# Kernel tuning notes

Hardware: AMD Instinct MI355X
Metric: run time of the kernel (lower is better)

## Reference

```python
import jax, jax.numpy as jnp
import numpy as np

EPS = 1e-12  # matches torch F.normalize eps


def _l2n(x, axis):
    return x / jnp.maximum(jnp.linalg.norm(x, axis=axis, keepdims=True), EPS)


def setup_inputs() -> dict:
    key = jax.random.key(0)
    k1, k2, k3 = jax.random.split(key, 3)
    x = jax.random.normal(k1, (4, 128, 30, 40), dtype=jnp.float32)
    conv_w = jax.random.normal(k2, (64, 128), dtype=jnp.float32) * 0.02  # 1x1 conv, no bias (vladv2=False)
    centroids = jax.random.uniform(k3, (64, 128), dtype=jnp.float32)
    return {"x": x, "conv_w": conv_w, "centroids": centroids}


def reference(x, conv_w, centroids):
    N, C, H, W = x.shape
    K = centroids.shape[0]
    ps, stride = 4, 1  # patch_sizes='4', strides='1'

    # descriptor-wise L2 normalization of input
    x = _l2n(x, 1)

    # 1x1 conv + softmax over clusters -> soft assignment [N,K,H,W]
    soft_assign = jax.nn.softmax(jnp.einsum('kc,nchw->nkhw', conv_w, x), axis=1)

    # weighted residuals [N,K,C,H,W] (vectorized form of the per-cluster loop)
    res = (x[:, None] - centroids[None, :, :, None, None]) * soft_assign[:, :, None]

    # global VLAD: sum over spatial, intra-norm, flatten, L2-norm
    vlad_global = res.sum(axis=(-1, -2))            # [N,K,C]
    vlad_global = _l2n(vlad_global, 2).reshape(N, K * C)
    vlad_global = _l2n(vlad_global, 1)

    # integral image over spatial dims with zero pad on top/left
    r = res.reshape(N, K * C, H, W)
    integ = jnp.cumsum(jnp.cumsum(r, axis=-1), axis=-2)
    integ = jnp.pad(integ, ((0, 0), (0, 0), (1, 0), (1, 0)))  # [N,KC,H+1,W+1]

    # dilated 2x2 box-filter conv == 4-corner integral-image lookup
    TL = integ[:, :, :H + 1 - ps:stride, :W + 1 - ps:stride]
    TR = integ[:, :, :H + 1 - ps:stride, ps::stride]
    BL = integ[:, :, ps::stride, :W + 1 - ps:stride]
    BR = integ[:, :, ps::stride, ps::stride]
    vl = (TL - TR - BL + BR) / (ps * ps)            # [N,KC,Hp,Wp]
    Hp, Wp = vl.shape[-2], vl.shape[-1]

    # local VLAD: intra-norm over descriptor dim, then global L2 per patch
    vl = vl.reshape(N, K, C, Hp * Wp)
    vl = _l2n(vl, 2).reshape(N, K * C, Hp * Wp)
    vlad_local = _l2n(vl, 1)

    return vlad_global, vlad_local
```

## Files before the change

kernel.cpp:

```cpp
#include <hip/hip_runtime.h>
#include <math.h>

#define EPSV 1e-12f

namespace {
constexpr int N_  = 4;
constexpr int C_  = 128;
constexpr int H_  = 30;
constexpr int W_  = 40;
constexpr int K_  = 64;
constexpr int HW_ = H_ * W_;
constexpr int HP_ = 27;
constexpr int WP_ = 37;
constexpr int P_  = HP_ * WP_;
constexpr int PS_ = 1000;
constexpr int KC_ = K_ * C_;
constexpr int CP_ = C_ * P_;
constexpr int CS_ = HP_ * W_;
constexpr int SL_ = CS_ / 4;
constexpr int CVP_ = 132;
}

static __device__ __forceinline__ float4 ld4(const float* p) {
    return *reinterpret_cast<const float4*>(p);
}
static __device__ __forceinline__ float dot4(float4 a, float4 b) {
    return a.x * b.x + a.y * b.y + a.z * b.z + a.w * b.w;
}
static __device__ __forceinline__ float4 f4add(float4 a, float4 b) {
    return make_float4(a.x + b.x, a.y + b.y, a.z + b.z, a.w + b.w);
}

__global__ __launch_bounds__(256) void k1_norm_softmax(
    const float* __restrict__ x, const float* __restrict__ conv_w,
    float* __restrict__ xnT, float* __restrict__ xnP, float* __restrict__ sa)
{
    __shared__ float xrow[C_ * W_];
    __shared__ float conv_s[K_ * CVP_];
    __shared__ float xrowT[W_ * CVP_];
    __shared__ float invn[W_];
    __shared__ float s_s[K_ * W_];

    const int b = blockIdx.x;
    const int n = b / H_, h = b - n * H_;
    const int t = threadIdx.x;

    for (int i = t; i < C_ * W_; i += 256) {
        const int c = i / W_, w = i - c * W_;
        xrow[i] = x[(size_t)(n * C_ + c) * HW_ + h * W_ + w];
    }
    for (int i = t; i < K_ * C_; i += 256) {
        const int k = i >> 7, c = i & 127;
        conv_s[k * CVP_ + c] = conv_w[i];
    }
    __syncthreads();

    if (t < W_) {
        float s = 0.f;
        for (int c = 0; c < C_; ++c) { const float v = xrow[c * W_ + t]; s += v * v; }
        invn[t] = 1.f / fmaxf(sqrtf(s), EPSV);
    }
    __syncthreads();

    for (int i = t; i < C_ * W_; i += 256) {
        const int c = i / W_, w = i - c * W_;
        const float v = xrow[i] * invn[w];
        xrow[i] = v;
        xnT[(size_t)(n * C_ + c) * HW_ + h * W_ + w] = v;
    }
    __syncthreads();

    for (int i = t; i < W_ * C_; i += 256) {
        const int w = i / C_, c = i - w * C_;
        const float v = xrow[c * W_ + w];
        xnP[((size_t)n * HW_ + h * W_ + w) * C_ + c] = v;
        xrowT[w * CVP_ + c] = v;
    }
    __syncthreads();

    {
        const int k = t >> 2, q = t & 3;
        float acc0 = 0.f, acc1 = 0.f, acc2 = 0.f, acc3 = 0.f, acc4 = 0.f;
        float acc5 = 0.f, acc6 = 0.f, acc7 = 0.f, acc8 = 0.f, acc9 = 0.f;
        const float* convk = &conv_s[k * CVP_];
        for (int ch = 0; ch < 4; ++ch) {
            float4 cv0 = ld4(convk + ch * 32 + 0),  cv1 = ld4(convk + ch * 32 + 4);
            float4 cv2 = ld4(convk + ch * 32 + 8),  cv3 = ld4(convk + ch * 32 + 12);
            float4 cv4 = ld4(convk + ch * 32 + 16), cv5 = ld4(convk + ch * 32 + 20);
            float4 cv6 = ld4(convk + ch * 32 + 24), cv7 = ld4(convk + ch * 32 + 28);
#pragma unroll
            for (int wi = 0; wi < 10; ++wi) {
                const float* xw = &xrowT[(q * 10 + wi) * CVP_ + ch * 32];
                float s = dot4(cv0, ld4(xw)) + dot4(cv1, ld4(xw + 4))
                        + dot4(cv2, ld4(xw + 8)) + dot4(cv3, ld4(xw + 12))
                        + dot4(cv4, ld4(xw + 16)) + dot4(cv5, ld4(xw + 20))
                        + dot4(cv6, ld4(xw + 24)) + dot4(cv7, ld4(xw + 28));
                if      (wi == 0) acc0 += s; else if (wi == 1) acc1 += s;
                else if (wi == 2) acc2 += s; else if (wi == 3) acc3 += s;
                else if (wi == 4) acc4 += s; else if (wi == 5) acc5 += s;
                else if (wi == 6) acc6 += s; else if (wi == 7) acc7 += s;
                else if (wi == 8) acc8 += s; else              acc9 += s;
            }
        }
        float* sd = &s_s[k * W_ + q * 10];
        sd[0] = acc0; sd[1] = acc1; sd[2] = acc2; sd[3] = acc3; sd[4] = acc4;
        sd[5] = acc5; sd[6] = acc6; sd[7] = acc7; sd[8] = acc8; sd[9] = acc9;
    }
    __syncthreads();

    if (t < W_) {
        const int w = t;
        float m = -1e30f;
        for (int k = 0; k < K_; ++k) m = fmaxf(m, s_s[k * W_ + w]);
        float sum = 0.f;
        for (int k = 0; k < K_; ++k) sum += expf(s_s[k * W_ + w] - m);
        const float inv = 1.f / sum;
        for (int k = 0; k < K_; ++k)
            sa[(size_t)(n * K_ + k) * HW_ + h * W_ + w] = expf(s_s[k * W_ + w] - m) * inv;
    }
}

#define COLSUM_VEC_T(cs_q, sa_s, x0, x1, x2, x3)                                \
    for (int s = t; s < SL_; s += 256) {                                        \
        const int i = s * 4;                                                    \
        const float4 sa0 = ld4(&sa_s[i]);                                       \
        const float4 sa1 = ld4(&sa_s[i + W_]);                                  \
        const float4 sa2 = ld4(&sa_s[i + 2 * W_]);                              \
        const float4 sa3 = ld4(&sa_s[i + 3 * W_]);                              \
        float acc[4][4];                                                        \
        const float* xc[4] = {x0, x1, x2, x3};                                  \
        _Pragma("unroll")                                                       \
        for (int ch = 0; ch < 4; ++ch) {                                        \
            const float4 a0 = ld4(xc[ch] + i);                                  \
            const float4 a1 = ld4(xc[ch] + i + W_);                             \
            const float4 a2 = ld4(xc[ch] + i + 2 * W_);                         \
            const float4 a3 = ld4(xc[ch] + i + 3 * W_);                         \
            acc[0][ch] = sa0.x * a0.x + sa1.x * a1.x + sa2.x * a2.x + sa3.x * a3.x; \
            acc[1][ch] = sa0.y * a0.y + sa1.y * a1.y + sa2.y * a2.y + sa3.y * a3.y; \
            acc[2][ch] = sa0.z * a0.z + sa1.z * a1.z + sa2.z * a2.z + sa3.z * a3.z; \
            acc[3][ch] = sa0.w * a0.w + sa1.w * a1.w + sa2.w * a2.w + sa3.w * a3.w; \
        }                                                                       \
        _Pragma("unroll")                                                       \
        for (int q = 0; q < 4; ++q)                                             \
            cs_q[q][s] = make_float4(acc[q][0], acc[q][1], acc[q][2], acc[q][3]); \
    }

#define WINDOW10(cs_q, b0, d, A0, A1, A2, A3)                                   \
    {                                                                           \
        float4 v0 = cs_q[(b0 + 0) & 3][(b0 + 0) >> 2];                          \
        float4 v1 = cs_q[(b0 + 1) & 3][(b0 + 1) >> 2];                          \
        float4 v2 = cs_q[(b0 + 2) & 3][(b0 + 2) >> 2];                          \
        float4 v3 = cs_q[(b0 + 3) & 3][(b0 + 3) >> 2];                          \
        float4 v4 = cs_q[(b0 + 4) & 3][(b0 + 4) >> 2];                          \
        float4 v5 = cs_q[(b0 + 5) & 3][(b0 + 5) >> 2];                          \
        float4 v6 = cs_q[(b0 + 6) & 3][(b0 + 6) >> 2];                          \
        float4 v7 = cs_q[(b0 + 7) & 3][(b0 + 7) >> 2];                          \
        float4 v8 = cs_q[(b0 + 8) & 3][(b0 + 8) >> 2];                          \
        float4 v9 = cs_q[(b0 + 9) & 3][(b0 + 9) >> 2];                          \
        const float4 t0 = f4add(v0, v1), t1 = f4add(v1, v2), t2 = f4add(v2, v3);\
        const float4 t3 = f4add(v3, v4), t4 = f4add(v4, v5), t5 = f4add(v5, v6);\
        const float4 t6 = f4add(v6, v7), t7 = f4add(v7, v8), t8 = f4add(v8, v9);\
        const float4 w0 = f4add(t0, t2), w1 = f4add(t1, t3), w2 = f4add(t2, t4);\
        const float4 w3 = f4add(t3, t5), w4 = f4add(t4, t6), w5 = f4add(t5, t7);\
        const float4 w6 = f4add(t6, t8);                                        \
        A0 = (0 < d) ? w0 : w3;                                                 \
        A1 = (1 < d) ? w1 : w4;                                                 \
        A2 = (2 < d) ? w2 : w5;                                                 \
        A3 = (3 < d) ? w3 : w6;                                                 \
    }

__global__ __launch_bounds__(256) void k4_merged(
    const float* __restrict__ sa, const float* __restrict__ xnT,
    const float* __restrict__ xnP, const float* __restrict__ cent,
    float* __restrict__ nsqp, float* __restrict__ vg_u,
    float* __restrict__ vg_r)
{
    __shared__ float  sa_s[HW_ + 8];
    __shared__ float4 cs_q[4][SL_ + 1];
    __shared__ float  gs[256], bss[256];
    __shared__ float  red[2];

    const int t = threadIdx.x;

    if (blockIdx.x < 256) {
        const int b = blockIdx.x;
        const int n = b >> 6, k = b & 63;
        const int c = t & 127, half = t >> 7;
        constexpr int HHW = HW_ / 2;

        const float* sarow = &sa[(size_t)b * HW_ + half * HHW];
        const float* xp = &xnP[((size_t)n * HW_ + half * HHW) * C_ + c];
        float g0 = 0.f, g1 = 0.f, g2 = 0.f, g3 = 0.f;
        float b0 = 0.f, b1 = 0.f, b2 = 0.f, b3 = 0.f;
        for (int pix = 0; pix < HHW; pix += 4) {
            const float s0 = sarow[pix + 0], s1 = sarow[pix + 1];
            const float s2 = sarow[pix + 2], s3 = sarow[pix + 3];
            g0 += s0 * xp[(size_t)(pix + 0) * C_];
            g1 += s1 * xp[(size_t)(pix + 1) * C_];
            g2 += s2 * xp[(size_t)(pix + 2) * C_];
            g3 += s3 * xp[(size_t)(pix + 3) * C_];
            b0 += s0; b1 += s1; b2 += s2; b3 += s3;
        }
        gs[t]  = (g0 + g1) + (g2 + g3);
        bss[t] = (b0 + b1) + (b2 + b3);
        __syncthreads();

        float vg = 0.f;
        if (t < 128) {
            vg = (gs[t] + gs[t + 128]) - cent[k * C_ + c] * (bss[t] + bss[t + 128]);
            float nsq = vg * vg;
            for (int off = 32; off >= 1; off >>= 1) nsq += __shfl_down(nsq, off);
            if ((t & 63) == 0) red[t >> 6] = nsq;
        }
        __syncthreads();
        const float tot  = red[0] + red[1];
        const float norm = sqrtf(tot);
        const float iv   = 1.f / fmaxf(norm, EPSV);
        if (t < 128) vg_u[(size_t)b * C_ + t] = vg * iv;
        if (t == 0) { const float rr = norm * iv; vg_r[b] = rr * rr; }
        return;
    }

    const int b  = blockIdx.x - 256;
    const int cq = b & 3;
    const int nk = b >> 2;
    const int n  = nk >> 6, k = nk & 63;

    for (int i = t; i < HW_; i += 256) sa_s[i] = sa[(size_t)nk * HW_ + i];
    __syncthreads();

    int hp0 = 0, b0 = 0, d = 4;
    float B0 = 0.f, B1 = 0.f, B2 = 0.f, B3 = 0.f;
    if (t < 250) {
        const int p0 = 4 * t;
        hp0 = p0 / WP_;
        const int wp0 = p0 - hp0 * WP_;
        b0 = p0 + 3 * hp0;
        d  = WP_ - wp0;
        const float* r0 = &sa_s[hp0 * W_ + wp0];
        float sc[10];
#pragma unroll
        for (int j = 0; j < 10; ++j)
            sc[j] = r0[j] + r0[j + W_] + r0[j + 2 * W_] + r0[j + 3 * W_];
        const float u0 = sc[0] + sc[1], u1 = sc[1] + sc[2], u2 = sc[2] + sc[3];
        const float u3 = sc[3] + sc[4], u4 = sc[4] + sc[5], u5 = sc[5] + sc[6];
        const float u6 = sc[6] + sc[7], u7 = sc[7] + sc[8], u8 = sc[8] + sc[9];
        const float wB0 = u0 + u2, wB1 = u1 + u3, wB2 = u2 + u4;
        const float wB3 = u3 + u5, wB4 = u4 + u6, wB5 = u5 + u7, wB6 = u6 + u8;
        B0 = (0 < d) ? wB0 : wB3;
        B1 = (1 < d) ? wB1 : wB4;
        B2 = (2 < d) ? wB2 : wB5;
        B3 = (3 < d) ? wB3 : wB6;
    }

    float4 nv0 = make_float4(0, 0, 0, 0), nv1 = nv0, nv2 = nv0, nv3 = nv0;
    const float* xb = xnT + (size_t)n * C_ * HW_;

    for (int g = 0; g < 8; ++g) {
        const int c0 = cq * 32 + g * 4;
        const float* x0 = xb + (size_t)(c0 + 0) * HW_;
        const float* x1 = xb + (size_t)(c0 + 1) * HW_;
        const float* x2 = xb + (size_t)(c0 + 2) * HW_;
        const float* x3 = xb + (size_t)(c0 + 3) * HW_;
        __syncthreads();
        COLSUM_VEC_T(cs_q, sa_s, x0, x1, x2, x3)
        __syncthreads();
        if (t < 250) {
            const float4 ce = ld4(&cent[k * C_ + c0]);
            float4 A0, A1, A2, A3;
            WINDOW10(cs_q, b0, d, A0, A1, A2, A3)
            const float4 e0 = make_float4(A0.x - ce.x * B0, A0.y - ce.y * B0,
                                          A0.z - ce.z * B0, A0.w - ce.w * B0);
            const float4 e1 = make_float4(A1.x - ce.x * B1, A1.y - ce.y * B1,
                                          A1.z - ce.z * B1, A1.w - ce.w * B1);
            const float4 e2 = make_float4(A2.x - ce.x * B2, A2.y - ce.y * B2,
                                          A2.z - ce.z * B2, A2.w - ce.w * B2);
            const float4 e3 = make_float4(A3.x - ce.x * B3, A3.y - ce.y * B3,
                                          A3.z - ce.z * B3, A3.w - ce.w * B3);
            nv0 = make_float4(nv0.x + e0.x * e0.x, nv0.y + e0.y * e0.y,
                              nv0.z + e0.z * e0.z, nv0.w + e0.w * e0.w);
            nv1 = make_float4(nv1.x + e1.x * e1.x, nv1.y + e1.y * e1.y,
                              nv1.z + e1.z * e1.z, nv1.w + e1.w * e1.w);
            nv2 = make_float4(nv2.x + e2.x * e2.x, nv2.y + e2.y * e2.y,
                              nv2.z + e2.z * e2.z, nv2.w + e2.w * e2.w);
            nv3 = make_float4(nv3.x + e3.x * e3.x, nv3.y + e3.y * e3.y,
                              nv3.z + e3.z * e3.z, nv3.w + e3.w * e3.w);
        }
    }
    if (t < 250) {
        const float s0 = (nv0.x + nv0.y) + (nv0.z + nv0.w);
        const float s1 = (nv1.x + nv1.y) + (nv1.z + nv1.w);
        const float s2 = (nv2.x + nv2.y) + (nv2.z + nv2.w);
        const float s3 = (nv3.x + nv3.y) + (nv3.z + nv3.w);
        *reinterpret_cast<float4*>(&nsqp[(size_t)b * PS_ + 4 * t]) =
            make_float4(s0 * 0.00390625f, s1 * 0.00390625f,
                        s2 * 0.00390625f, s3 * 0.00390625f);
    }
}

__global__ __launch_bounds__(256) void k5_merged(
    const float* __restrict__ nsqp, float* __restrict__ inv1,
    float* __restrict__ rloc, const float* __restrict__ vg_u,
    const float* __restrict__ vg_r, float* __restrict__ out)
{
    const int t = threadIdx.x;
    if (blockIdx.x >= 256) {
        const int n = blockIdx.x - 256;
        __shared__ float inv2s;
        if (t == 0) {
            float s = 0.f;
            for (int k = 0; k < K_; ++k) s += vg_r[n * K_ + k];
            inv2s = 1.f / fmaxf(sqrtf(s), EPSV);
        }
        __syncthreads();
        const float inv2 = inv2s;
        for (int i = t; i < KC_; i += 256)
            out[(size_t)n * KC_ + i] = vg_u[(size_t)n * KC_ + i] * inv2;
        return;
    }
    const int nk = blockIdx.x;
    if (t < 250) {
        const int p0 = 4 * t;
        const float4 a = ld4(&nsqp[(size_t)(nk * 4 + 0) * PS_ + p0]);
        const float4 b = ld4(&nsqp[(size_t)(nk * 4 + 1) * PS_ + p0]);
        const float4 c = ld4(&nsqp[(size_t)(nk * 4 + 2) * PS_ + p0]);
        const float4 e = ld4(&nsqp[(size_t)(nk * 4 + 3) * PS_ + p0]);
        float4 iv, rr;
#pragma unroll
        for (int j = 0; j < 4; ++j) {
            const float s = reinterpret_cast<const float*>(&a)[j]
                          + reinterpret_cast<const float*>(&b)[j]
                          + reinterpret_cast<const float*>(&c)[j]
                          + reinterpret_cast<const float*>(&e)[j];
            const float norm = sqrtf(s);
            const float v = 1.f / fmaxf(norm, EPSV);
            reinterpret_cast<float*>(&iv)[j] = v * 0.0625f;
            const float r = norm * v;
            reinterpret_cast<float*>(&rr)[j] = r * r;
        }
        *reinterpret_cast<float4*>(&inv1[(size_t)nk * PS_ + p0]) = iv;
        *reinterpret_cast<float4*>(&rloc[(size_t)nk * PS_ + p0]) = rr;
    }
}

__global__ __launch_bounds__(256) void k6_inv2(
    const float* __restrict__ rloc, float* __restrict__ inv2)
{
    const int n = blockIdx.x;
    const int t = threadIdx.x;
    if (t < 250) {
        const int p0 = 4 * t;
        float4 s = make_float4(0, 0, 0, 0);
        for (int k = 0; k < K_; ++k) {
            const float4 r = ld4(&rloc[(size_t)(n * K_ + k) * PS_ + p0]);
            s = f4add(s, r);
        }
        float4 o;
        o.x = 1.f / fmaxf(sqrtf(s.x), EPSV);
        o.y = 1.f / fmaxf(sqrtf(s.y), EPSV);
        o.z = 1.f / fmaxf(sqrtf(s.z), EPSV);
        o.w = 1.f / fmaxf(sqrtf(s.w), EPSV);
        *reinterpret_cast<float4*>(&inv2[n * PS_ + p0]) = o;
    }
}

__global__ __launch_bounds__(256) void k7_write(
    const float* __restrict__ sa, const float* __restrict__ xnT,
    const float* __restrict__ cent, const float* __restrict__ inv1,
    const float* __restrict__ inv2, float* __restrict__ outl)
{
    __shared__ float  sa_s[HW_ + 8];
    __shared__ float  scl_s[P_];
    __shared__ float  t2_s[P_];
    __shared__ float4 cs_q[4][SL_ + 1];

    const int b  = blockIdx.x;
    const int cq = b & 3;
    const int nk = b >> 2;
    const int n  = nk >> 6, k = nk & 63;
    const int t  = threadIdx.x;

    for (int i = t; i < HW_; i += 256) sa_s[i] = sa[(size_t)nk * HW_ + i];
    __syncthreads();
    for (int p = t; p < P_; p += 256) {
        const int hp = p / WP_, wp = p - hp * WP_;
        float bs = 0.f;
#pragma unroll
        for (int dh = 0; dh < 4; ++dh) {
            const float* r = &sa_s[(hp + dh) * W_ + wp];
            bs += r[0] + r[1] + r[2] + r[3];
        }
        const float sc = inv1[(size_t)nk * PS_ + p] * inv2[n * PS_ + p];
        scl_s[p] = sc;
        t2_s[p]  = bs * sc;
    }

    const float* xb = xnT + (size_t)n * C_ * HW_;
    float* ob = outl + (size_t)nk * CP_;

    for (int g = 0; g < 8; ++g) {
        const int m = g & 3, h8 = g >> 2;
        const int c0 = cq * 32 + h8 * 16 + m;
        const float* x0 = xb + (size_t)(c0 + 0) * HW_;
        const float* x1 = xb + (size_t)(c0 + 4) * HW_;
        const float* x2 = xb + (size_t)(c0 + 8) * HW_;
        const float* x3 = xb + (size_t)(c0 + 12) * HW_;
        __syncthreads();
        COLSUM_VEC_T(cs_q, sa_s, x0, x1, x2, x3)
        __syncthreads();
        const float ce0 = cent[k * C_ + c0];
        const float ce1 = cent[k * C_ + c0 + 4];
        const float ce2 = cent[k * C_ + c0 + 8];
        const float ce3 = cent[k * C_ + c0 + 12];
        float* ob0 = ob + (size_t)(c0 + 0) * P_;
        float* ob1 = ob + (size_t)(c0 + 4) * P_;
        float* ob2 = ob + (size_t)(c0 + 8) * P_;
        float* ob3 = ob + (size_t)(c0 + 12) * P_;

        if (t < 249) {
            const int p0 = m + 4 * t;
            const int hp0 = p0 / WP_;
            const int wp0 = p0 - hp0 * WP_;
            const int b0 = p0 + 3 * hp0;
            const int d  = WP_ - wp0;
            const float sc0 = scl_s[p0 + 0], sc1 = scl_s[p0 + 1];
            const float sc2 = scl_s[p0 + 2], sc3 = scl_s[p0 + 3];
            const float tt0 = t2_s[p0 + 0], tt1 = t2_s[p0 + 1];
            const float tt2 = t2_s[p0 + 2], tt3 = t2_s[p0 + 3];
            float4 A0, A1, A2, A3;
            WINDOW10(cs_q, b0, d, A0, A1, A2, A3)
            const float4 s0v = make_float4(A0.x * sc0 - ce0 * tt0, A1.x * sc1 - ce0 * tt1,
                                           A2.x * sc2 - ce0 * tt2, A3.x * sc3 - ce0 * tt3);
            const float4 s1v = make_float4(A0.y * sc0 - ce1 * tt0, A1.y * sc1 - ce1 * tt1,
                                           A2.y * sc2 - ce1 * tt2, A3.y * sc3 - ce1 * tt3);
            const float4 s2v = make_float4(A0.z * sc0 - ce2 * tt0, A1.z * sc1 - ce2 * tt1,
                                           A2.z * sc2 - ce2 * tt2, A3.z * sc3 - ce2 * tt3);
            const float4 s3v = make_float4(A0.w * sc0 - ce3 * tt0, A1.w * sc1 - ce3 * tt1,
                                           A2.w * sc2 - ce3 * tt2, A3.w * sc3 - ce3 * tt3);
            *reinterpret_cast<float4*>(ob0 + p0) = s0v;
            *reinterpret_cast<float4*>(ob1 + p0) = s1v;
            *reinterpret_cast<float4*>(ob2 + p0) = s2v;
            *reinterpret_cast<float4*>(ob3 + p0) = s3v;
        } else if (t < 252) {
            const int u = t - 249;
            const int p = (u < m) ? u : 996 + u;
            const int hp = p / WP_, wp = p - hp * WP_;
            const int base = hp * W_ + wp;
            const float4 s0 = cs_q[(base + 0) & 3][(base + 0) >> 2];
            const float4 s1 = cs_q[(base + 1) & 3][(base + 1) >> 2];
            const float4 s2 = cs_q[(base + 2) & 3][(base + 2) >> 2];
            const float4 s3 = cs_q[(base + 3) & 3][(base + 3) >> 2];
            const float sc = scl_s[p], tt = t2_s[p];
            ob0[p] = (s0.x + s1.x + s2.x + s3.x) * sc - ce0 * tt;
            ob1[p] = (s0.y + s1.y + s2.y + s3.y) * sc - ce1 * tt;
            ob2[p] = (s0.z + s1.z + s2.z + s3.z) * sc - ce2 * tt;
            ob3[p] = (s0.w + s1.w + s2.w + s3.w) * sc - ce3 * tt;
        }
    }
}

extern "C" void kernel_launch(void* const* d_in, const int* in_sizes, int n_in,
                              void* d_out, int out_size, void* d_ws, size_t ws_size,
                              hipStream_t stream)
{
    const float* x      = (const float*)d_in[0];
    const float* conv_w = (const float*)d_in[1];
    const float* cent   = (const float*)d_in[2];
    float* out = (float*)d_out;
    float* ws  = (float*)d_ws;

    float* xnT  = ws;
    float* xnP  = ws + 614400;
    float* sa   = ws + 1228800;
    float* vg_u = ws + 1536000;
    float* vg_r = ws + 1568768;
    float* nsqp = ws + 1569024;
    float* inv1 = ws + 2593024;
    float* rloc = ws + 2849024;
    float* inv2 = ws + 3105024;

    float* outl = out + (size_t)N_ * KC_;

    k1_norm_softmax<<<N_ * H_, 256, 0, stream>>>(x, conv_w, xnT, xnP, sa);
    k4_merged<<<256 + N_ * K_ * 4, 256, 0, stream>>>(sa, xnT, xnP, cent,
                                                     nsqp, vg_u, vg_r);
    k5_merged<<<256 + N_, 256, 0, stream>>>(nsqp, inv1, rloc, vg_u, vg_r, out);
    k6_inv2<<<N_, 256, 0, stream>>>(rloc, inv2);
    k7_write<<<N_ * K_ * 4, 256, 0, stream>>>(sa, xnT, cent, inv1, inv2, outl);
}
```

Before: 120.2 us.

## Replace shared-memory colsum/window passes with per-thread register 2x4 patch tiles

The k4 and k7 box-filter kernels no longer stage soft-assignments and column sums in shared memory with block barriers. Each thread now owns a 2-row by 4-column group of output patches and reads a 5x8 window of sa and xnT straight from global memory into registers, computing the 4x4 box sums locally for each channel in its slice. This removes every __syncthreads and the shared-memory staging, and spreads the work over a flat grid of threads. The cost is redundant overlapping global loads (each input element is read by several threads), possibly uncoalesced unaligned stores, and more register use per thread.

```diff
diff --git a/kernel.cpp b/kernel.cpp
--- a/kernel.cpp
+++ b/kernel.cpp
@@ -16,19 +16,31 @@
 constexpr int PS_ = 1000;
 constexpr int KC_ = K_ * C_;
 constexpr int CP_ = C_ * P_;
-constexpr int CS_ = HP_ * W_;
-constexpr int SL_ = CS_ / 4;
 constexpr int CVP_ = 132;
-}
+constexpr int SLOT_ = 140;
+constexpr int K4S_BLK = 560;
+constexpr int K7_BLK  = 1120;
+}
+
+typedef float4 f4u __attribute__((aligned(4)));
 
 static __device__ __forceinline__ float4 ld4(const float* p) {
     return *reinterpret_cast<const float4*>(p);
 }
+static __device__ __forceinline__ float4 ld4u(const float* p) {
+    return *reinterpret_cast<const f4u*>(p);
+}
+static __device__ __forceinline__ void st4u(float* p, float4 v) {
+    *reinterpret_cast<f4u*>(p) = v;
+}
 static __device__ __forceinline__ float dot4(float4 a, float4 b) {
     return a.x * b.x + a.y * b.y + a.z * b.z + a.w * b.w;
 }
 static __device__ __forceinline__ float4 f4add(float4 a, float4 b) {
     return make_float4(a.x + b.x, a.y + b.y, a.z + b.z, a.w + b.w);
+}
+static __device__ __forceinline__ float4 f4mul(float4 a, float4 b) {
+    return make_float4(a.x * b.x, a.y * b.y, a.z * b.z, a.w * b.w);
 }
 
 __global__ __launch_bounds__(256) void k1_norm_softmax(
@@ -80,8 +92,7 @@
 
     {
         const int k = t >> 2, q = t & 3;
-        float acc0 = 0.f, acc1 = 0.f, acc2 = 0.f, acc3 = 0.f, acc4 = 0.f;
-        float acc5 = 0.f, acc6 = 0.f, acc7 = 0.f, acc8 = 0.f, acc9 = 0.f;
+        float acc[10] = {};
         const float* convk = &conv_s[k * CVP_];
         for (int ch = 0; ch < 4; ++ch) {
             float4 cv0 = ld4(convk + ch * 32 + 0),  cv1 = ld4(convk + ch * 32 + 4);
@@ -91,20 +102,15 @@
 #pragma unroll
             for (int wi = 0; wi < 10; ++wi) {
                 const float* xw = &xrowT[(q * 10 + wi) * CVP_ + ch * 32];
-                float s = dot4(cv0, ld4(xw)) + dot4(cv1, ld4(xw + 4))
-                        + dot4(cv2, ld4(xw + 8)) + dot4(cv3, ld4(xw + 12))
-                        + dot4(cv4, ld4(xw + 16)) + dot4(cv5, ld4(xw + 20))
-                        + dot4(cv6, ld4(xw + 24)) + dot4(cv7, ld4(xw + 28));
-                if      (wi == 0) acc0 += s; else if (wi == 1) acc1 += s;
-                else if (wi == 2) acc2 += s; else if (wi == 3) acc3 += s;
-                else if (wi == 4) acc4 += s; else if (wi == 5) acc5 += s;
-                else if (wi == 6) acc6 += s; else if (wi == 7) acc7 += s;
-                else if (wi == 8) acc8 += s; else              acc9 += s;
+                acc[wi] += dot4(cv0, ld4(xw)) + dot4(cv1, ld4(xw + 4))
+                         + dot4(cv2, ld4(xw + 8)) + dot4(cv3, ld4(xw + 12))
+                         + dot4(cv4, ld4(xw + 16)) + dot4(cv5, ld4(xw + 20))
+                         + dot4(cv6, ld4(xw + 24)) + dot4(cv7, ld4(xw + 28));
             }
         }
         float* sd = &s_s[k * W_ + q * 10];
-        sd[0] = acc0; sd[1] = acc1; sd[2] = acc2; sd[3] = acc3; sd[4] = acc4;
-        sd[5] = acc5; sd[6] = acc6; sd[7] = acc7; sd[8] = acc8; sd[9] = acc9;
+#pragma unroll
+        for (int wi = 0; wi < 10; ++wi) sd[wi] = acc[wi];
     }
     __syncthreads();
 
@@ -120,70 +126,23 @@
     }
 }
 
-#define COLSUM_VEC_T(cs_q, sa_s, x0, x1, x2, x3)                                \
-    for (int s = t; s < SL_; s += 256) {                                        \
-        const int i = s * 4;                                                    \
-        const float4 sa0 = ld4(&sa_s[i]);                                       \
-        const float4 sa1 = ld4(&sa_s[i + W_]);                                  \
-        const float4 sa2 = ld4(&sa_s[i + 2 * W_]);                              \
-        const float4 sa3 = ld4(&sa_s[i + 3 * W_]);                              \
-        float acc[4][4];                                                        \
-        const float* xc[4] = {x0, x1, x2, x3};                                  \
-        _Pragma("unroll")                                                       \
-        for (int ch = 0; ch < 4; ++ch) {                                        \
-            const float4 a0 = ld4(xc[ch] + i);                                  \
-            const float4 a1 = ld4(xc[ch] + i + W_);                             \
-            const float4 a2 = ld4(xc[ch] + i + 2 * W_);                         \
-            const float4 a3 = ld4(xc[ch] + i + 3 * W_);                         \
-            acc[0][ch] = sa0.x * a0.x + sa1.x * a1.x + sa2.x * a2.x + sa3.x * a3.x; \
-            acc[1][ch] = sa0.y * a0.y + sa1.y * a1.y + sa2.y * a2.y + sa3.y * a3.y; \
-            acc[2][ch] = sa0.z * a0.z + sa1.z * a1.z + sa2.z * a2.z + sa3.z * a3.z; \
-            acc[3][ch] = sa0.w * a0.w + sa1.w * a1.w + sa2.w * a2.w + sa3.w * a3.w; \
-        }                                                                       \
-        _Pragma("unroll")                                                       \
-        for (int q = 0; q < 4; ++q)                                             \
-            cs_q[q][s] = make_float4(acc[q][0], acc[q][1], acc[q][2], acc[q][3]); \
-    }
-
-#define WINDOW10(cs_q, b0, d, A0, A1, A2, A3)                                   \
-    {                                                                           \
-        float4 v0 = cs_q[(b0 + 0) & 3][(b0 + 0) >> 2];                          \
-        float4 v1 = cs_q[(b0 + 1) & 3][(b0 + 1) >> 2];                          \
-        float4 v2 = cs_q[(b0 + 2) & 3][(b0 + 2) >> 2];                          \
-        float4 v3 = cs_q[(b0 + 3) & 3][(b0 + 3) >> 2];                          \
-        float4 v4 = cs_q[(b0 + 4) & 3][(b0 + 4) >> 2];                          \
-        float4 v5 = cs_q[(b0 + 5) & 3][(b0 + 5) >> 2];                          \
-        float4 v6 = cs_q[(b0 + 6) & 3][(b0 + 6) >> 2];                          \
-        float4 v7 = cs_q[(b0 + 7) & 3][(b0 + 7) >> 2];                          \
-        float4 v8 = cs_q[(b0 + 8) & 3][(b0 + 8) >> 2];                          \
-        float4 v9 = cs_q[(b0 + 9) & 3][(b0 + 9) >> 2];                          \
-        const float4 t0 = f4add(v0, v1), t1 = f4add(v1, v2), t2 = f4add(v2, v3);\
-        const float4 t3 = f4add(v3, v4), t4 = f4add(v4, v5), t5 = f4add(v5, v6);\
-        const float4 t6 = f4add(v6, v7), t7 = f4add(v7, v8), t8 = f4add(v8, v9);\
-        const float4 w0 = f4add(t0, t2), w1 = f4add(t1, t3), w2 = f4add(t2, t4);\
-        const float4 w3 = f4add(t3, t5), w4 = f4add(t4, t6), w5 = f4add(t5, t7);\
-        const float4 w6 = f4add(t6, t8);                                        \
-        A0 = (0 < d) ? w0 : w3;                                                 \
-        A1 = (1 < d) ? w1 : w4;                                                 \
-        A2 = (2 < d) ? w2 : w5;                                                 \
-        A3 = (3 < d) ? w3 : w6;                                                 \
-    }
-
-__global__ __launch_bounds__(256) void k4_merged(
+static __device__ __forceinline__ float4 win4(float4 a, float4 b) {
+    const float t0 = a.x + a.y, t1 = a.y + a.z, t2 = a.z + a.w;
+    const float t3 = a.w + b.x, t4 = b.x + b.y, t5 = b.y + b.z;
+    return make_float4(t0 + t2, t1 + t3, t2 + t4, t3 + t5);
+}
+
+__global__ __launch_bounds__(256) void k4_flat(
     const float* __restrict__ sa, const float* __restrict__ xnT,
     const float* __restrict__ xnP, const float* __restrict__ cent,
     float* __restrict__ nsqp, float* __restrict__ vg_u,
     float* __restrict__ vg_r)
 {
-    __shared__ float  sa_s[HW_ + 8];
-    __shared__ float4 cs_q[4][SL_ + 1];
-    __shared__ float  gs[256], bss[256];
-    __shared__ float  red[2];
-
+    __shared__ float gs[256], bss[256], red[2];
     const int t = threadIdx.x;
 
-    if (blockIdx.x < 256) {
-        const int b = blockIdx.x;
+    if (blockIdx.x >= K4S_BLK) {
+        const int b = blockIdx.x - K4S_BLK;
         const int n = b >> 6, k = b & 63;
         const int c = t & 127, half = t >> 7;
         constexpr int HHW = HW_ / 2;
@@ -221,80 +180,74 @@
         return;
     }
 
-    const int b  = blockIdx.x - 256;
-    const int cq = b & 3;
-    const int nk = b >> 2;
-    const int n  = nk >> 6, k = nk & 63;
-
-    for (int i = t; i < HW_; i += 256) sa_s[i] = sa[(size_t)nk * HW_ + i];
-    __syncthreads();
-
-    int hp0 = 0, b0 = 0, d = 4;
-    float B0 = 0.f, B1 = 0.f, B2 = 0.f, B3 = 0.f;
-    if (t < 250) {
-        const int p0 = 4 * t;
-        hp0 = p0 / WP_;
-        const int wp0 = p0 - hp0 * WP_;
-        b0 = p0 + 3 * hp0;
-        d  = WP_ - wp0;
-        const float* r0 = &sa_s[hp0 * W_ + wp0];
-        float sc[10];
-#pragma unroll
-        for (int j = 0; j < 10; ++j)
-            sc[j] = r0[j] + r0[j + W_] + r0[j + 2 * W_] + r0[j + 3 * W_];
-        const float u0 = sc[0] + sc[1], u1 = sc[1] + sc[2], u2 = sc[2] + sc[3];
-        const float u3 = sc[3] + sc[4], u4 = sc[4] + sc[5], u5 = sc[5] + sc[6];
-        const float u6 = sc[6] + sc[7], u7 = sc[7] + sc[8], u8 = sc[8] + sc[9];
-        const float wB0 = u0 + u2, wB1 = u1 + u3, wB2 = u2 + u4;
-        const float wB3 = u3 + u5, wB4 = u4 + u6, wB5 = u5 + u7, wB6 = u6 + u8;
-        B0 = (0 < d) ? wB0 : wB3;
-        B1 = (1 < d) ? wB1 : wB4;
-        B2 = (2 < d) ? wB2 : wB5;
-        B3 = (3 < d) ? wB3 : wB6;
-    }
-
-    float4 nv0 = make_float4(0, 0, 0, 0), nv1 = nv0, nv2 = nv0, nv3 = nv0;
-    const float* xb = xnT + (size_t)n * C_ * HW_;
-
-    for (int g = 0; g < 8; ++g) {
-        const int c0 = cq * 32 + g * 4;
-        const float* x0 = xb + (size_t)(c0 + 0) * HW_;
-        const float* x1 = xb + (size_t)(c0 + 1) * HW_;
-        const float* x2 = xb + (size_t)(c0 + 2) * HW_;
-        const float* x3 = xb + (size_t)(c0 + 3) * HW_;
-        __syncthreads();
-        COLSUM_VEC_T(cs_q, sa_s, x0, x1, x2, x3)
-        __syncthreads();
-        if (t < 250) {
-            const float4 ce = ld4(&cent[k * C_ + c0]);
-            float4 A0, A1, A2, A3;
-            WINDOW10(cs_q, b0, d, A0, A1, A2, A3)
-            const float4 e0 = make_float4(A0.x - ce.x * B0, A0.y - ce.y * B0,
-                                          A0.z - ce.z * B0, A0.w - ce.w * B0);
-            const float4 e1 = make_float4(A1.x - ce.x * B1, A1.y - ce.y * B1,
-                                          A1.z - ce.z * B1, A1.w - ce.w * B1);
-            const float4 e2 = make_float4(A2.x - ce.x * B2, A2.y - ce.y * B2,
-                                          A2.z - ce.z * B2, A2.w - ce.w * B2);
-            const float4 e3 = make_float4(A3.x - ce.x * B3, A3.y - ce.y * B3,
-                                          A3.z - ce.z * B3, A3.w - ce.w * B3);
-            nv0 = make_float4(nv0.x + e0.x * e0.x, nv0.y + e0.y * e0.y,
-                              nv0.z + e0.z * e0.z, nv0.w + e0.w * e0.w);
-            nv1 = make_float4(nv1.x + e1.x * e1.x, nv1.y + e1.y * e1.y,
-                              nv1.z + e1.z * e1.z, nv1.w + e1.w * e1.w);
-            nv2 = make_float4(nv2.x + e2.x * e2.x, nv2.y + e2.y * e2.y,
-                              nv2.z + e2.z * e2.z, nv2.w + e2.w * e2.w);
-            nv3 = make_float4(nv3.x + e3.x * e3.x, nv3.y + e3.y * e3.y,
-                              nv3.z + e3.z * e3.z, nv3.w + e3.w * e3.w);
-        }
-    }
-    if (t < 250) {
-        const float s0 = (nv0.x + nv0.y) + (nv0.z + nv0.w);
-        const float s1 = (nv1.x + nv1.y) + (nv1.z + nv1.w);
-        const float s2 = (nv2.x + nv2.y) + (nv2.z + nv2.w);
-        const float s3 = (nv3.x + nv3.y) + (nv3.z + nv3.w);
-        *reinterpret_cast<float4*>(&nsqp[(size_t)b * PS_ + 4 * t]) =
-            make_float4(s0 * 0.00390625f, s1 * 0.00390625f,
-                        s2 * 0.00390625f, s3 * 0.00390625f);
+    const int id   = blockIdx.x * 256 + t;
+    const int nkcq = id / SLOT_;
+    const int item = id - nkcq * SLOT_;
+    const int cq = nkcq & 3, nk = nkcq >> 2;
+    const int n  = nk >> 6,  k  = nk & 63;
+    const int hq = item / 10, wq = item - hq * 10;
+    const int h0 = 2 * hq;
+    const int nrow = (hq < 13) ? 2 : 1;
+    const int w0 = 4 * wq;
+
+    const float* sab = sa + (size_t)nk * HW_;
+    float4 s0[5], s1[5];
+#pragma unroll
+    for (int r = 0; r < 5; ++r) {
+        s0[r] = ld4(sab + (h0 + r) * W_ + w0);
+        s1[r] = ld4(sab + (h0 + r) * W_ + w0 + 4);
+    }
+    float4 Bv[2];
+    {
+        const float4 m123a = f4add(f4add(s0[1], s0[2]), s0[3]);
+        const float4 m123b = f4add(f4add(s1[1], s1[2]), s1[3]);
+        Bv[0] = win4(f4add(s0[0], m123a), f4add(s1[0], m123b));
+        Bv[1] = win4(f4add(m123a, s0[4]), f4add(m123b, s1[4]));
+    }
+
+    float4 nsq0 = make_float4(0, 0, 0, 0), nsq1 = nsq0;
+    const float* xb = xnT + (size_t)n * C_ * HW_ + h0 * W_ + w0;
+    const float* ck = cent + k * C_;
+
+    for (int ci = 0; ci < 32; ++ci) {
+        const int c = cq * 32 + ci;
+        const float* xr = xb + (size_t)c * HW_;
+        float4 pA[5], pB[5];
+#pragma unroll
+        for (int r = 0; r < 5; ++r) {
+            pA[r] = f4mul(s0[r], ld4(xr + r * W_));
+            pB[r] = f4mul(s1[r], ld4(xr + r * W_ + 4));
+        }
+        const float4 m123a = f4add(f4add(pA[1], pA[2]), pA[3]);
+        const float4 m123b = f4add(f4add(pB[1], pB[2]), pB[3]);
+        const float4 A0 = win4(f4add(pA[0], m123a), f4add(pB[0], m123b));
+        const float4 A1 = win4(f4add(m123a, pA[4]), f4add(m123b, pB[4]));
+        const float cc = ck[c];
+        const float e00 = A0.x - cc * Bv[0].x, e01 = A0.y - cc * Bv[0].y;
+        const float e02 = A0.z - cc * Bv[0].z, e03 = A0.w - cc * Bv[0].w;
+        const float e10 = A1.x - cc * Bv[1].x, e11 = A1.y - cc * Bv[1].y;
+        const float e12 = A1.z - cc * Bv[1].z, e13 = A1.w - cc * Bv[1].w;
+        nsq0.x += e00 * e00; nsq0.y += e01 * e01; nsq0.z += e02 * e02; nsq0.w += e03 * e03;
+        nsq1.x += e10 * e10; nsq1.y += e11 * e11; nsq1.z += e12 * e12; nsq1.w += e13 * e13;
+    }
+
+    const float sc16 = 0.00390625f;
+    float* np = nsqp + (size_t)(nk * 4 + cq) * PS_;
+    {
+        const int p = WP_ * h0 + w0;
+        if (wq < 9)
+            st4u(np + p, make_float4(nsq0.x * sc16, nsq0.y * sc16,
+                                     nsq0.z * sc16, nsq0.w * sc16));
+        else
+            np[p] = nsq0.x * sc16;
+    }
+    if (nrow == 2) {
+        const int p = WP_ * (h0 + 1) + w0;
+        if (wq < 9)
+            st4u(np + p, make_float4(nsq1.x * sc16, nsq1.y * sc16,
+                                     nsq1.z * sc16, nsq1.w * sc16));
+        else
+            np[p] = nsq1.x * sc16;
     }
 }
 
@@ -364,97 +317,78 @@
     }
 }
 
-__global__ __launch_bounds__(256) void k7_write(
+__global__ __launch_bounds__(256) void k7_flat(
     const float* __restrict__ sa, const float* __restrict__ xnT,
     const float* __restrict__ cent, const float* __restrict__ inv1,
     const float* __restrict__ inv2, float* __restrict__ outl)
 {
-    __shared__ float  sa_s[HW_ + 8];
-    __shared__ float  scl_s[P_];
-    __shared__ float  t2_s[P_];
-    __shared__ float4 cs_q[4][SL_ + 1];
-
-    const int b  = blockIdx.x;
-    const int cq = b & 3;
-    const int nk = b >> 2;
-    const int n  = nk >> 6, k = nk & 63;
-    const int t  = threadIdx.x;
-
-    for (int i = t; i < HW_; i += 256) sa_s[i] = sa[(size_t)nk * HW_ + i];
-    __syncthreads();
-    for (int p = t; p < P_; p += 256) {
-        const int hp = p / WP_, wp = p - hp * WP_;
-        float bs = 0.f;
-#pragma unroll
-        for (int dh = 0; dh < 4; ++dh) {
-            const float* r = &sa_s[(hp + dh) * W_ + wp];
-            bs += r[0] + r[1] + r[2] + r[3];
-        }
-        const float sc = inv1[(size_t)nk * PS_ + p] * inv2[n * PS_ + p];
-        scl_s[p] = sc;
-        t2_s[p]  = bs * sc;
-    }
-
-    const float* xb = xnT + (size_t)n * C_ * HW_;
+    const int id   = blockIdx.x * 256 + threadIdx.x;
+    const int nkcq = id / SLOT_;
+    const int item = id - nkcq * SLOT_;
+    const int cq8 = nkcq & 7, nk = nkcq >> 3;
+    const int n  = nk >> 6,  k  = nk & 63;
+    const int hq = item / 10, wq = item - hq * 10;
+    const int h0 = 2 * hq;
+    const int nrow = (hq < 13) ? 2 : 1;
+    const int w0 = 4 * wq;
+
+    const float* sab = sa + (size_t)nk * HW_;
+    float4 s0[5], s1[5];
+#pragma unroll
+    for (int r = 0; r < 5; ++r) {
+        s0[r] = ld4(sab + (h0 + r) * W_ + w0);
+        s1[r] = ld4(sab + (h0 + r) * W_ + w0 + 4);
+    }
+    float4 Bv[2];
+    {
+        const float4 m123a = f4add(f4add(s0[1], s0[2]), s0[3]);
+        const float4 m123b = f4add(f4add(s1[1], s1[2]), s1[3]);
+        Bv[0] = win4(f4add(s0[0], m123a), f4add(s1[0], m123b));
+        Bv[1] = win4(f4add(m123a, s0[4]), f4add(m123b, s1[4]));
+    }
+
+    const int p0r0 = WP_ * h0 + w0;
+    const int p0r1 = WP_ * (h0 + 1) + w0;
+    const float4 sc0 = f4mul(ld4u(inv1 + (size_t)nk * PS_ + p0r0),
+                             ld4u(inv2 + (size_t)n * PS_ + p0r0));
+    const float4 sc1 = f4mul(ld4u(inv1 + (size_t)nk * PS_ + p0r1),
+                             ld4u(inv2 + (size_t)n * PS_ + p0r1));
+    const float4 tt0 = f4mul(Bv[0], sc0);
+    const float4 tt1 = f4mul(Bv[1], sc1);
+
+    const float* xb = xnT + (size_t)n * C_ * HW_ + h0 * W_ + w0;
+    const float* ck = cent + k * C_;
     float* ob = outl + (size_t)nk * CP_;
 
-    for (int g = 0; g < 8; ++g) {
-        const int m = g & 3, h8 = g >> 2;
-        const int c0 = cq * 32 + h8 * 16 + m;
-        const float* x0 = xb + (size_t)(c0 + 0) * HW_;
-        const float* x1 = xb + (size_t)(c0 + 4) * HW_;
-        const float* x2 = xb + (size_t)(c0 + 8) * HW_;
-        const float* x3 = xb + (size_t)(c0 + 12) * HW_;
-        __syncthreads();
-        COLSUM_VEC_T(cs_q, sa_s, x0, x1, x2, x3)
-        __syncthreads();
-        const float ce0 = cent[k * C_ + c0];
-        const float ce1 = cent[k * C_ + c0 + 4];
-        const float ce2 = cent[k * C_ + c0 + 8];
-        const float ce3 = cent[k * C_ + c0 + 12];
-        float* ob0 = ob + (size_t)(c0 + 0) * P_;
-        float* ob1 = ob + (size_t)(c0 + 4) * P_;
-        float* ob2 = ob + (size_t)(c0 + 8) * P_;
-        float* ob3 = ob + (size_t)(c0 + 12) * P_;
-
-        if (t < 249) {
-            const int p0 = m + 4 * t;
-            const int hp0 = p0 / WP_;
-            const int wp0 = p0 - hp0 * WP_;
-            const int b0 = p0 + 3 * hp0;
-            const int d  = WP_ - wp0;
-            const float sc0 = scl_s[p0 + 0], sc1 = scl_s[p0 + 1];
-            const float sc2 = scl_s[p0 + 2], sc3 = scl_s[p0 + 3];
-            const float tt0 = t2_s[p0 + 0], tt1 = t2_s[p0 + 1];
-            const float tt2 = t2_s[p0 + 2], tt3 = t2_s[p0 + 3];
-            float4 A0, A1, A2, A3;
-            WINDOW10(cs_q, b0, d, A0, A1, A2, A3)
-            const float4 s0v = make_float4(A0.x * sc0 - ce0 * tt0, A1.x * sc1 - ce0 * tt1,
-                                           A2.x * sc2 - ce0 * tt2, A3.x * sc3 - ce0 * tt3);
-            const float4 s1v = make_float4(A0.y * sc0 - ce1 * tt0, A1.y * sc1 - ce1 * tt1,
-                                           A2.y * sc2 - ce1 * tt2, A3.y * sc3 - ce1 * tt3);
-            const float4 s2v = make_float4(A0.z * sc0 - ce2 * tt0, A1.z * sc1 - ce2 * tt1,
-                                           A2.z * sc2 - ce2 * tt2, A3.z * sc3 - ce2 * tt3);
-            const float4 s3v = make_float4(A0.w * sc0 - ce3 * tt0, A1.w * sc1 - ce3 * tt1,
-                                           A2.w * sc2 - ce3 * tt2, A3.w * sc3 - ce3 * tt3);
-            *reinterpret_cast<float4*>(ob0 + p0) = s0v;
-            *reinterpret_cast<float4*>(ob1 + p0) = s1v;
-            *reinterpret_cast<float4*>(ob2 + p0) = s2v;
-            *reinterpret_cast<float4*>(ob3 + p0) = s3v;
-        } else if (t < 252) {
-            const int u = t - 249;
-            const int p = (u < m) ? u : 996 + u;
-            const int hp = p / WP_, wp = p - hp * WP_;
-            const int base = hp * W_ + wp;
-            const float4 s0 = cs_q[(base + 0) & 3][(base + 0) >> 2];
-            const float4 s1 = cs_q[(base + 1) & 3][(base + 1) >> 2];
-            const float4 s2 = cs_q[(base + 2) & 3][(base + 2) >> 2];
-            const float4 s3 = cs_q[(base + 3) & 3][(base + 3) >> 2];
-            const float sc = scl_s[p], tt = t2_s[p];
-            ob0[p] = (s0.x + s1.x + s2.x + s3.x) * sc - ce0 * tt;
-            ob1[p] = (s0.y + s1.y + s2.y + s3.y) * sc - ce1 * tt;
-            ob2[p] = (s0.z + s1.z + s2.z + s3.z) * sc - ce2 * tt;
-            ob3[p] = (s0.w + s1.w + s2.w + s3.w) * sc - ce3 * tt;
+    for (int ci = 0; ci < 16; ++ci) {
+        const int c = cq8 * 16 + ci;
+        const float* xr = xb + (size_t)c * HW_;
+        float4 pA[5], pB[5];
+#pragma unroll
+        for (int r = 0; r < 5; ++r) {
+            pA[r] = f4mul(s0[r], ld4(xr + r * W_));
+            pB[r] = f4mul(s1[r], ld4(xr + r * W_ + 4));
+        }
+        const float4 m123a = f4add(f4add(pA[1], pA[2]), pA[3]);
+        const float4 m123b = f4add(f4add(pB[1], pB[2]), pB[3]);
+        const float4 A0 = win4(f4add(pA[0], m123a), f4add(pB[0], m123b));
+        const float4 A1 = win4(f4add(m123a, pA[4]), f4add(m123b, pB[4]));
+        const float cc = ck[c];
+        float* oc = ob + (size_t)c * P_;
+        if (wq < 9) {
+            st4u(oc + p0r0, make_float4(A0.x * sc0.x - cc * tt0.x,
+                                        A0.y * sc0.y - cc * tt0.y,
+                                        A0.z * sc0.z - cc * tt0.z,
+                                        A0.w * sc0.w - cc * tt0.w));
+            if (nrow == 2)
+                st4u(oc + p0r1, make_float4(A1.x * sc1.x - cc * tt1.x,
+                                            A1.y * sc1.y - cc * tt1.y,
+                                            A1.z * sc1.z - cc * tt1.z,
+                                            A1.w * sc1.w - cc * tt1.w));
+        } else {
+            oc[p0r0] = A0.x * sc0.x - cc * tt0.x;
+            if (nrow == 2)
+                oc[p0r1] = A1.x * sc1.x - cc * tt1.x;
         }
     }
 }
@@ -482,9 +416,9 @@
     float* outl = out + (size_t)N_ * KC_;
 
     k1_norm_softmax<<<N_ * H_, 256, 0, stream>>>(x, conv_w, xnT, xnP, sa);
-    k4_merged<<<256 + N_ * K_ * 4, 256, 0, stream>>>(sa, xnT, xnP, cent,
-                                                     nsqp, vg_u, vg_r);
+    k4_flat<<<K4S_BLK + 256, 256, 0, stream>>>(sa, xnT, xnP, cent,
+                                               nsqp, vg_u, vg_r);
     k5_merged<<<256 + N_, 256, 0, stream>>>(nsqp, inv1, rloc, vg_u, vg_r, out);
     k6_inv2<<<N_, 256, 0, stream>>>(rloc, inv2);
-    k7_write<<<N_ * K_ * 4, 256, 0, stream>>>(sa, xnT, cent, inv1, inv2, outl);
-}
+    k7_flat<<<K7_BLK, 256, 0, stream>>>(sa, xnT, cent, inv1, inv2, outl);
+}
```

Result: slower. 122.9 us (+2.3%).
